# Kernel optimization log

Hardware: AMD Instinct MI355X
Metric: run time of the kernel (lower is better)

The kernel has to match this reference:

```python
import jax, jax.numpy as jnp
import numpy as np

NUM_TYPES = 8
NUM_REL = 6
N_LAYERS = 2


def setup_inputs() -> dict:
    key = jax.random.key(0)
    ks = jax.random.split(key, 8)
    N, E, D_in, D = 20000, 320000, 512, 256
    node_feature = jax.random.normal(ks[0], (N, D_in), dtype=jnp.float32)
    node_type = jax.random.randint(ks[1], (N,), 0, NUM_TYPES)
    edge_index = jax.random.randint(ks[2], (2, E), 0, N)
    edge_type = jax.random.randint(ks[3], (E,), 0, NUM_REL)
    node_position = jnp.arange(N)
    # learned params
    adapt_W = jax.random.normal(ks[4], (NUM_TYPES, D, D_in), dtype=jnp.float32) * 0.02
    adapt_b = jnp.zeros((NUM_TYPES, D), dtype=jnp.float32)
    W_rel = jax.random.normal(ks[5], (N_LAYERS, NUM_REL, D, D), dtype=jnp.float32) * 0.05
    W_self = jax.random.normal(ks[6], (N_LAYERS, D, D), dtype=jnp.float32) * 0.05
    b_self = jnp.zeros((N_LAYERS, D), dtype=jnp.float32)
    return {
        "node_feature": node_feature,
        "node_type": node_type,
        "edge_index": edge_index,
        "edge_type": edge_type,
        "node_position": node_position,
        "adapt_W": adapt_W,
        "adapt_b": adapt_b,
        "W_rel": W_rel,
        "W_self": W_self,
        "b_self": b_self,
    }


def reference(node_feature, node_type, edge_index, edge_type, node_position,
              adapt_W, adapt_b, W_rel, W_self, b_self):
    N = node_feature.shape[0]
    D = adapt_W.shape[1]
    # per-node-type adaptation: res[i] = tanh(W_{t_i} x_i + b_{t_i})
    # (original loops over types with boolean gather/scatter; here we mask-select)
    h = jnp.zeros((N, D), dtype=node_feature.dtype)
    for t in range(NUM_TYPES):
        y = jnp.tanh(node_feature @ adapt_W[t].T + adapt_b[t])
        h = jnp.where((node_type == t)[:, None], y, h)
    # dropout p=0.0 -> identity
    src, dst = edge_index[0], edge_index[1]
    deg = jax.ops.segment_sum(jnp.ones(src.shape, h.dtype), dst, num_segments=N)
    inv_deg = (1.0 / jnp.maximum(deg, 1.0))[:, None]  # [N,1]
    # relational GNN layer stack (stand-in for unseen GraphConv)
    for l in range(N_LAYERS):
        hr = jnp.einsum('nd,rde->rne', h, W_rel[l])      # [R,N,D]
        msg = hr[edge_type, src]                          # [E,D] gather by (relation, src)
        agg = jax.ops.segment_sum(msg, dst, num_segments=N)
        h = jax.nn.relu(agg * inv_deg + h @ W_self[l] + b_self[l])
    return h
```

## Files before the change

kernel.cpp:

```cpp
#include <hip/hip_runtime.h>

constexpr int NTYPES = 8;
constexpr int NREL   = 6;
constexpr int NSLOT  = 7;
constexpr int D      = 256;
constexpr int DIN    = 512;
constexpr int LDH    = NSLOT * D;

using short8 = __attribute__((ext_vector_type(8))) short;
using f32x4  = __attribute__((ext_vector_type(4))) float;

__device__ __forceinline__ ushort f2b(float f) {
  unsigned u = __float_as_uint(f);
  u += 0x7fffu + ((u >> 16) & 1u);
  return (ushort)(u >> 16);
}
__device__ __forceinline__ float b2f(unsigned bits16) {
  return __uint_as_float(bits16 << 16);
}

#define GLOAD_LDS16(g, l)                                              \
  __builtin_amdgcn_global_load_lds(                                    \
      (__attribute__((address_space(1))) void*)(g),                    \
      (__attribute__((address_space(3))) void*)(l), 16, 0, 0)

__global__ void k_zero(int* __restrict__ p, int n) {
  int i = blockIdx.x * blockDim.x + threadIdx.x;
  if (i < n) p[i] = 0;
}

__global__ void k_cvt_bf16(const float* __restrict__ in, ushort* __restrict__ out, int n4) {
  int i = blockIdx.x * blockDim.x + threadIdx.x;
  if (i >= n4) return;
  float4 v = ((const float4*)in)[i];
  ushort4 o;
  o.x = f2b(v.x); o.y = f2b(v.y); o.z = f2b(v.z); o.w = f2b(v.w);
  ((ushort4*)out)[i] = o;
}

__global__ void k_pack_wcat(const float* __restrict__ Wrel, const float* __restrict__ Wself,
                            ushort* __restrict__ Wcat) {
  int l = blockIdx.z, s = blockIdx.y;
  int o = blockIdx.x * 256 + threadIdx.x;
  int e = o >> 8, d = o & 255;
  float v = (s < NREL) ? Wrel[(((size_t)l * NREL + s) * D + d) * D + e]
                       : Wself[((size_t)l * D + d) * D + e];
  Wcat[(((size_t)l * NSLOT + s) * D + e) * D + d] = f2b(v);
}

__global__ void k_type_blockcnt(const int* __restrict__ ntype, int* __restrict__ blockcnt,
                                int N) {
  __shared__ int cnt[NTYPES];
  int i = blockIdx.x * 256 + threadIdx.x;
  if (threadIdx.x < NTYPES) cnt[threadIdx.x] = 0;
  __syncthreads();
  int t = (i < N) ? ntype[i] : -1;
#pragma unroll
  for (int ty = 0; ty < NTYPES; ++ty) {
    unsigned long long m = __ballot(t == ty);
    if ((threadIdx.x & 63) == 0 && m) atomicAdd(&cnt[ty], __popcll(m));
  }
  __syncthreads();
  if (threadIdx.x < NTYPES) blockcnt[blockIdx.x * NTYPES + threadIdx.x] = cnt[threadIdx.x];
}

__global__ void k_type_scan(const int* __restrict__ blockcnt, int* __restrict__ boffset,
                            int* __restrict__ cnt, int* __restrict__ offt, int nb) {
  __shared__ int tot[NTYPES];
  __shared__ int base[NTYPES];
  int t = threadIdx.x;
  if (t < NTYPES) {
    int s = 0;
    for (int b = 0; b < nb; ++b) {
      boffset[b * NTYPES + t] = s;
      s += blockcnt[b * NTYPES + t];
    }
    tot[t] = s;
    cnt[t] = s;
  }
  __syncthreads();
  if (t == 0) {
    int s = 0;
    for (int ty = 0; ty < NTYPES; ++ty) { base[ty] = s; offt[ty] = s; s += tot[ty]; }
  }
  __syncthreads();
  if (t < NTYPES)
    for (int b = 0; b < nb; ++b) boffset[b * NTYPES + t] += base[t];
}

__global__ void k_type_scatter(const int* __restrict__ ntype, const int* __restrict__ boffset,
                               int* __restrict__ perm, int N) {
  __shared__ int cur[NTYPES];
  int i = blockIdx.x * 256 + threadIdx.x;
  if (threadIdx.x < NTYPES) cur[threadIdx.x] = boffset[blockIdx.x * NTYPES + threadIdx.x];
  __syncthreads();
  int t = (i < N) ? ntype[i] : -1;
  int lane = threadIdx.x & 63;
#pragma unroll
  for (int ty = 0; ty < NTYPES; ++ty) {
    unsigned long long m = __ballot(t == ty);
    if (m) {
      int wbase = 0;
      if (lane == 0) wbase = atomicAdd(&cur[ty], __popcll(m));
      wbase = __shfl(wbase, 0);
      if (t == ty) {
        int rank = __popcll(m & ((1ull << lane) - 1ull));
        perm[wbase + rank] = i;
      }
    }
  }
}

__global__ void k_degree(const int* __restrict__ dst, int* deg, int E) {
  int i = blockIdx.x * blockDim.x + threadIdx.x;
  if (i < E) atomicAdd(&deg[dst[i]], 1);
}

__global__ void k_scan_block(const int* __restrict__ deg, int* __restrict__ rowptr,
                             int* __restrict__ bsum, int N) {
  __shared__ int s[256];
  int i = blockIdx.x * 256 + threadIdx.x;
  int v = (i < N) ? deg[i] : 0;
  s[threadIdx.x] = v;
  __syncthreads();
  for (int o = 1; o < 256; o <<= 1) {
    int t = (threadIdx.x >= o) ? s[threadIdx.x - o] : 0;
    __syncthreads();
    s[threadIdx.x] += t;
    __syncthreads();
  }
  if (i < N) rowptr[i] = s[threadIdx.x] - v;
  if (threadIdx.x == 255) bsum[blockIdx.x] = s[255];
}
__global__ void k_scan_bsum(int* bsum, int nb) {
  if (threadIdx.x == 0) {
    int s = 0;
    for (int b = 0; b < nb; ++b) { int t = bsum[b]; bsum[b] = s; s += t; }
  }
}
__global__ void k_scan_add(int* __restrict__ rowptr, int* __restrict__ cursor,
                           const int* __restrict__ bsum, const int* __restrict__ deg,
                           float* __restrict__ inv, int N, int E) {
  int i = blockIdx.x * 256 + threadIdx.x;
  if (i < N) {
    int r = rowptr[i] + bsum[blockIdx.x];
    rowptr[i] = r;
    cursor[i] = r;
    inv[i] = 1.0f / fmaxf((float)deg[i], 1.0f);
  }
  if (i == 0) rowptr[N] = E;
}
__global__ void k_sortedges(const int* __restrict__ src, const int* __restrict__ dst,
                            const int* __restrict__ et, int* cursor,
                            int* __restrict__ epack, int E) {
  int e = blockIdx.x * 256 + threadIdx.x;
  if (e < E) {
    int pos = atomicAdd(&cursor[dst[e]], 1);
    epack[pos] = (src[e] << 3) | et[e];
  }
}

template <int BM, int BN, int NTN, int KDIM, bool ADAPT, int OCC>
__global__ __launch_bounds__(256, OCC)
void k_mfma_gemm(const ushort* __restrict__ A, const ushort* __restrict__ B,
                 const float* __restrict__ bias,
                 const int* __restrict__ perm, const int* __restrict__ cnt,
                 const int* __restrict__ off,
                 ushort* __restrict__ Cout, int N, int ldC) {
  const int nwg = gridDim.x;
  const int qq = nwg >> 3, rr = nwg & 7;
  const int xcd = blockIdx.x & 7, idx = blockIdx.x >> 3;
  const int wgid = (xcd < rr ? xcd * (qq + 1) : rr * (qq + 1) + (xcd - rr) * qq) + idx;

  int mcnt = N, mtile, ntile;
  const int* permt = nullptr;
  const ushort* Bt = B;
  const float* biast = bias;
  if (ADAPT) {
    const int mt = nwg / (NTYPES * NTN);
    const int t = wgid / (mt * NTN);
    const int rem = wgid % (mt * NTN);
    mtile = rem / NTN;
    ntile = rem % NTN;
    mcnt = cnt[t];
    permt = perm + off[t];
    Bt = B + (size_t)t * D * KDIM;
    biast = bias + t * D;
  } else {
    mtile = wgid / NTN;
    ntile = wgid % NTN;
  }
  const int m0 = mtile * BM;
  if (m0 >= mcnt) return;
  const int n0 = ntile * BN;

  __shared__ ushort SM[2][2][BM * 32];
  static_assert(BM * BN <= 2 * 2 * BM * 32, "C tile must fit in staging LDS");

  const int tid  = threadIdx.x;
  const int lane = tid & 63;
  const int w    = tid >> 6;
  constexpr int FR = BM / 32;
  constexpr int FC = BN / 32;
  const int wr   = (w >> 1) * (BM / 2);
  const int wc   = (w & 1) * (BN / 2);

  constexpr int PW = BM / 16 / 4;
  const ushort* gA[PW];
  const ushort* gB[PW];
  int lo[PW];
#pragma unroll
  for (int u = 0; u < PW; ++u) {
    const int c  = w + u * 4;
    const int r  = c * 16 + (lane >> 2);
    const int sl = (lane & 3) ^ ((r >> 1) & 3);
    int ga;
    if (ADAPT) ga = permt[min(m0 + r, mcnt - 1)];
    else       ga = min(m0 + r, N - 1);
    gA[u] = A + (size_t)ga * KDIM + sl * 8;
    gB[u] = Bt + (size_t)(n0 + r) * KDIM + sl * 8;
    lo[u] = c * 512;
  }

  auto STAGE = [&](int k0, int buf) {
#pragma unroll
    for (int u = 0; u < PW; ++u) {
      GLOAD_LDS16(gA[u] + k0, &SM[buf][0][lo[u]]);
      GLOAD_LDS16(gB[u] + k0, &SM[buf][1][lo[u]]);
    }
  };

  f32x4 acc[FR][FC] = {};

  const int r15 = lane & 15;
  const int g   = lane >> 4;
  const int gsw = g ^ ((r15 >> 1) & 3);

  STAGE(0, 0);
  __syncthreads();

  constexpr int NT = KDIM / 32;
  int curb = 0;
#pragma unroll
  for (int kt = 0; kt < NT; ++kt) {
    if (kt + 1 < NT) STAGE((kt + 1) * 32, curb ^ 1);

    short8 af[FR], bf[FC];
#pragma unroll
    for (int i = 0; i < FR; ++i)
      af[i] = *(const short8*)(&SM[curb][0][(wr + i * 16 + r15) * 32 + gsw * 8]);
#pragma unroll
    for (int j = 0; j < FC; ++j)
      bf[j] = *(const short8*)(&SM[curb][1][(wc + j * 16 + r15) * 32 + gsw * 8]);
#pragma unroll
    for (int i = 0; i < FR; ++i)
#pragma unroll
      for (int j = 0; j < FC; ++j)
        acc[i][j] = __builtin_amdgcn_mfma_f32_16x16x32_bf16(af[i], bf[j], acc[i][j], 0, 0, 0);

    __syncthreads();
    curb ^= 1;
  }

  ushort* Ct = (ushort*)SM;
#pragma unroll
  for (int i = 0; i < FR; ++i) {
#pragma unroll
    for (int q4 = 0; q4 < 4; ++q4) {
      const int row = wr + i * 16 + (lane >> 4) * 4 + q4;
#pragma unroll
      for (int j = 0; j < FC; ++j) {
        const int col = wc + j * 16 + r15;
        float v = acc[i][j][q4];
        if (ADAPT) v = tanhf(v + biast[n0 + col]);
        Ct[row * BN + col] = f2b(v);
      }
    }
  }
  __syncthreads();
  constexpr int C8 = BN / 8;
  constexpr int UNITS = BM * C8;
#pragma unroll
  for (int u0 = 0; u0 < UNITS; u0 += 256) {
    const int u = u0 + tid;
    const int row = u / C8, c8 = u % C8;
    const int rl = m0 + row;
    if (rl < mcnt) {
      const int grow = ADAPT ? permt[rl] : rl;
      *(short8*)(Cout + (size_t)grow * ldC + n0 + c8 * 8) =
          *(const short8*)(Ct + row * BN + c8 * 8);
    }
  }
}

template <bool LAST>
__global__ void k_combine(const ushort* __restrict__ Hall, const int* __restrict__ rowptr,
                          const int* __restrict__ epack, const float* __restrict__ invd,
                          const float* __restrict__ bias, void* __restrict__ outp, int N) {
  int v = blockIdx.x * 4 + (threadIdx.x >> 6);
  if (v >= N) return;
  int lane = threadIdx.x & 63;
  int e0 = rowptr[v], e1 = rowptr[v + 1];
  const uint2 s = *(const uint2*)(Hall + (size_t)v * LDH + NREL * D + lane * 4);
  float iv = invd[v];
  const float4 b4 = *(const float4*)(bias + lane * 4);

  float a0 = 0.f, a1 = 0.f, a2 = 0.f, a3 = 0.f;
  int e = e0;
  for (; e + 8 <= e1; e += 8) {
    uint2 u[8];
#pragma unroll
    for (int k = 0; k < 8; ++k) {
      int p = epack[e + k];
      u[k] = *(const uint2*)(Hall + (size_t)(p >> 3) * LDH + (p & 7) * D + lane * 4);
    }
#pragma unroll
    for (int k = 0; k < 8; ++k) {
      a0 += b2f(u[k].x & 0xffffu);
      a1 += __uint_as_float(u[k].x & 0xffff0000u);
      a2 += b2f(u[k].y & 0xffffu);
      a3 += __uint_as_float(u[k].y & 0xffff0000u);
    }
  }
  if (e + 4 <= e1) {
    uint2 u[4];
#pragma unroll
    for (int k = 0; k < 4; ++k) {
      int p = epack[e + k];
      u[k] = *(const uint2*)(Hall + (size_t)(p >> 3) * LDH + (p & 7) * D + lane * 4);
    }
#pragma unroll
    for (int k = 0; k < 4; ++k) {
      a0 += b2f(u[k].x & 0xffffu);
      a1 += __uint_as_float(u[k].x & 0xffff0000u);
      a2 += b2f(u[k].y & 0xffffu);
      a3 += __uint_as_float(u[k].y & 0xffff0000u);
    }
    e += 4;
  }
  for (; e < e1; ++e) {
    int p = epack[e];
    const uint2 u = *(const uint2*)(Hall + (size_t)(p >> 3) * LDH + (p & 7) * D + lane * 4);
    a0 += b2f(u.x & 0xffffu);
    a1 += __uint_as_float(u.x & 0xffff0000u);
    a2 += b2f(u.y & 0xffffu);
    a3 += __uint_as_float(u.y & 0xffff0000u);
  }
  float o0 = fmaxf(fmaf(a0, iv, b2f(s.x & 0xffffu)) + b4.x, 0.f);
  float o1 = fmaxf(fmaf(a1, iv, __uint_as_float(s.x & 0xffff0000u)) + b4.y, 0.f);
  float o2 = fmaxf(fmaf(a2, iv, b2f(s.y & 0xffffu)) + b4.z, 0.f);
  float o3 = fmaxf(fmaf(a3, iv, __uint_as_float(s.y & 0xffff0000u)) + b4.w, 0.f);
  if (LAST) {
    float4 o; o.x = o0; o.y = o1; o.z = o2; o.w = o3;
    ((float4*)outp)[(size_t)v * 64 + lane] = o;
  } else {
    ushort4 o; o.x = f2b(o0); o.y = f2b(o1); o.z = f2b(o2); o.w = f2b(o3);
    ((ushort4*)outp)[(size_t)v * 64 + lane] = o;
  }
}

extern "C" void kernel_launch(void* const* d_in, const int* in_sizes, int n_in,
                              void* d_out, int out_size, void* d_ws, size_t ws_size,
                              hipStream_t stream) {
  const float* X       = (const float*)d_in[0];
  const int*   ntype   = (const int*)d_in[1];
  const int*   eidx    = (const int*)d_in[2];
  const int*   etype   = (const int*)d_in[3];
  const float* adapt_W = (const float*)d_in[5];
  const float* adapt_b = (const float*)d_in[6];
  const float* W_rel   = (const float*)d_in[7];
  const float* W_self  = (const float*)d_in[8];
  const float* b_self  = (const float*)d_in[9];

  const int N = in_sizes[1];
  const int E = in_sizes[3];
  const int* src = eidx;
  const int* dst = eidx + E;

  char* ws = (char*)d_ws;
  size_t o = 0;
  auto alloc = [&](size_t bytes) { void* p = ws + o; o += (bytes + 255) & ~255ull; return p; };

  ushort* Hall  = (ushort*)alloc((size_t)N * LDH * 2);
  ushort* Xb    = Hall;
  ushort* h     = (ushort*)alloc((size_t)N * D * 2);
  ushort* Wab   = (ushort*)alloc((size_t)NTYPES * D * DIN * 2);
  ushort* Wcat  = (ushort*)alloc((size_t)2 * NSLOT * D * D * 2);
  int*   deg    = (int*)alloc((size_t)N * 4);
  float* inv    = (float*)alloc((size_t)N * 4);
  int*   perm   = (int*)alloc((size_t)N * 4);
  int*   rowptr = (int*)alloc((size_t)(N + 1) * 4);
  int*   cursor = (int*)alloc((size_t)N * 4);
  int*   epack  = (int*)alloc((size_t)E * 4);
  int*   bsum   = (int*)alloc(1024 * 4);
  int*   blockcnt = (int*)alloc((size_t)1024 * NTYPES * 4);
  int*   boffset  = (int*)alloc((size_t)1024 * NTYPES * 4);
  int*   cnt    = (int*)alloc(NTYPES * 4);
  int*   offt   = (int*)alloc(NTYPES * 4);

  const int thr = 256;
  const int nbN = (N + thr - 1) / thr;
  const int nbE = (E + thr - 1) / thr;

  k_zero<<<nbN, thr, 0, stream>>>(deg, N);

  k_cvt_bf16<<<(N * DIN / 4 + thr - 1) / thr, thr, 0, stream>>>(X, Xb, N * DIN / 4);
  k_cvt_bf16<<<(NTYPES * D * DIN / 4 + thr - 1) / thr, thr, 0, stream>>>(adapt_W, Wab,
                                                                          NTYPES * D * DIN / 4);
  dim3 gW(D * D / 256, NSLOT, 2);
  k_pack_wcat<<<gW, 256, 0, stream>>>(W_rel, W_self, Wcat);

  k_type_blockcnt<<<nbN, thr, 0, stream>>>(ntype, blockcnt, N);
  k_type_scan<<<1, 64, 0, stream>>>(blockcnt, boffset, cnt, offt, nbN);
  k_type_scatter<<<nbN, thr, 0, stream>>>(ntype, boffset, perm, N);
  k_degree<<<nbE, thr, 0, stream>>>(dst, deg, E);

  k_scan_block<<<nbN, 256, 0, stream>>>(deg, rowptr, bsum, N);
  k_scan_bsum<<<1, 64, 0, stream>>>(bsum, nbN);
  k_scan_add<<<nbN, 256, 0, stream>>>(rowptr, cursor, bsum, deg, inv, N, E);
  k_sortedges<<<nbE, 256, 0, stream>>>(src, dst, etype, cursor, epack, E);

  const int mtA = (N + 63) / 64;
  const int nwgA = NTYPES * mtA * (D / 64);
  k_mfma_gemm<64, 64, D / 64, DIN, true, 6><<<nwgA, 256, 0, stream>>>(
      Xb, Wab, adapt_b, perm, cnt, offt, h, N, D);

  const int mtL = (N + 127) / 128;
  const int nwgL = mtL * (LDH / 128);
  for (int l = 0; l < 2; ++l) {
    const ushort* Wl = Wcat + (size_t)l * NSLOT * D * D;
    k_mfma_gemm<128, 128, LDH / 128, D, false, 4><<<nwgL, 256, 0, stream>>>(
        h, Wl, nullptr, nullptr, nullptr, nullptr, Hall, N, LDH);
    if (l == 0)
      k_combine<false><<<(N + 3) / 4, 256, 0, stream>>>(Hall, rowptr, epack, inv,
                                                        b_self + (size_t)l * D, h, N);
    else
      k_combine<true><<<(N + 3) / 4, 256, 0, stream>>>(Hall, rowptr, epack, inv,
                                                       b_self + (size_t)l * D, d_out, N);
  }
}
```

Baseline: 231.1 us.

## Aggregate neighbors per relation before transform, then one K=1792 GEMM

Reorders each GNN layer from transform-then-gather to gather-then-transform. A new aggregate kernel sums bf16 neighbor features per relation into a [N, 7*256] buffer scaled by inverse degree, with the self features in the last slot. A single GEMM against concatenated weights (K=1792, output 256) then applies bias and ReLU in its epilogue. This cuts the gather width from a 1792-wide Hall row to a 256-wide h row and removes the separate combine pass. The cost is 6 per-relation accumulators in registers, with a branch on relation type per edge, and a GEMM with a longer K.

```diff
diff --git a/kernel.cpp b/kernel.cpp
--- a/kernel.cpp
+++ b/kernel.cpp
@@ -38,14 +38,15 @@
   ((ushort4*)out)[i] = o;
 }
 
-__global__ void k_pack_wcat(const float* __restrict__ Wrel, const float* __restrict__ Wself,
-                            ushort* __restrict__ Wcat) {
-  int l = blockIdx.z, s = blockIdx.y;
-  int o = blockIdx.x * 256 + threadIdx.x;
-  int e = o >> 8, d = o & 255;
-  float v = (s < NREL) ? Wrel[(((size_t)l * NREL + s) * D + d) * D + e]
-                       : Wself[((size_t)l * D + d) * D + e];
-  Wcat[(((size_t)l * NSLOT + s) * D + e) * D + d] = f2b(v);
+__global__ void k_pack_wcat2(const float* __restrict__ Wrel, const float* __restrict__ Wself,
+                             ushort* __restrict__ W2) {
+  int l = blockIdx.y;
+  int idx = blockIdx.x * 256 + threadIdx.x;
+  int e = idx / LDH, k = idx % LDH;
+  float v = (k < NREL * D)
+                ? Wrel[(((size_t)l * NREL + (k >> 8)) * D + (k & 255)) * D + e]
+                : Wself[((size_t)l * D + (k - NREL * D)) * D + e];
+  W2[((size_t)l * D + e) * LDH + k] = f2b(v);
 }
 
 __global__ void k_type_blockcnt(const int* __restrict__ ntype, int* __restrict__ blockcnt,
@@ -160,13 +161,65 @@
   }
 }
 
-template <int BM, int BN, int NTN, int KDIM, bool ADAPT, int OCC>
+__global__ void k_aggregate(const ushort* __restrict__ h, const int* __restrict__ rowptr,
+                            const int* __restrict__ epack, const float* __restrict__ invd,
+                            ushort* __restrict__ S, int N) {
+  int v = blockIdx.x * 4 + (threadIdx.x >> 6);
+  if (v >= N) return;
+  int lane = threadIdx.x & 63;
+  float acc[NREL][4] = {};
+  int e0 = rowptr[v], e1 = rowptr[v + 1];
+
+  auto ACC = [&](int p, uint2 u) {
+    float f0 = b2f(u.x & 0xffffu), f1 = __uint_as_float(u.x & 0xffff0000u);
+    float f2 = b2f(u.y & 0xffffu), f3 = __uint_as_float(u.y & 0xffff0000u);
+    int r = __builtin_amdgcn_readfirstlane(p) & 7;
+    switch (r) {
+      case 0: acc[0][0]+=f0; acc[0][1]+=f1; acc[0][2]+=f2; acc[0][3]+=f3; break;
+      case 1: acc[1][0]+=f0; acc[1][1]+=f1; acc[1][2]+=f2; acc[1][3]+=f3; break;
+      case 2: acc[2][0]+=f0; acc[2][1]+=f1; acc[2][2]+=f2; acc[2][3]+=f3; break;
+      case 3: acc[3][0]+=f0; acc[3][1]+=f1; acc[3][2]+=f2; acc[3][3]+=f3; break;
+      case 4: acc[4][0]+=f0; acc[4][1]+=f1; acc[4][2]+=f2; acc[4][3]+=f3; break;
+      default: acc[5][0]+=f0; acc[5][1]+=f1; acc[5][2]+=f2; acc[5][3]+=f3; break;
+    }
+  };
+
+  int e = e0;
+  for (; e + 8 <= e1; e += 8) {
+    int p[8]; uint2 u[8];
+#pragma unroll
+    for (int k = 0; k < 8; ++k) {
+      p[k] = epack[e + k];
+      u[k] = *(const uint2*)(h + (size_t)(p[k] >> 3) * D + lane * 4);
+    }
+#pragma unroll
+    for (int k = 0; k < 8; ++k) ACC(p[k], u[k]);
+  }
+  for (; e < e1; ++e) {
+    int p = epack[e];
+    uint2 u = *(const uint2*)(h + (size_t)(p >> 3) * D + lane * 4);
+    ACC(p, u);
+  }
+
+  float iv = invd[v];
+#pragma unroll
+  for (int r = 0; r < NREL; ++r) {
+    ushort4 o;
+    o.x = f2b(acc[r][0] * iv); o.y = f2b(acc[r][1] * iv);
+    o.z = f2b(acc[r][2] * iv); o.w = f2b(acc[r][3] * iv);
+    *(ushort4*)(S + (size_t)v * LDH + r * D + lane * 4) = o;
+  }
+  uint2 sh = *(const uint2*)(h + (size_t)v * D + lane * 4);
+  *(uint2*)(S + (size_t)v * LDH + NREL * D + lane * 4) = sh;
+}
+
+template <int BM, int BN, int NTN, int KDIM, bool ADAPT, int EPI, int OCC>
 __global__ __launch_bounds__(256, OCC)
 void k_mfma_gemm(const ushort* __restrict__ A, const ushort* __restrict__ B,
                  const float* __restrict__ bias,
                  const int* __restrict__ perm, const int* __restrict__ cnt,
                  const int* __restrict__ off,
-                 ushort* __restrict__ Cout, int N, int ldC) {
+                 void* __restrict__ Cout, int N, int ldC) {
   const int nwg = gridDim.x;
   const int qq = nwg >> 3, rr = nwg & 7;
   const int xcd = blockIdx.x & 7, idx = blockIdx.x >> 3;
@@ -195,7 +248,7 @@
   const int n0 = ntile * BN;
 
   __shared__ ushort SM[2][2][BM * 32];
-  static_assert(BM * BN <= 2 * 2 * BM * 32, "C tile must fit in staging LDS");
+  static_assert(EPI == 2 || BM * BN <= 2 * 2 * BM * 32, "C tile must fit staging LDS");
 
   const int tid  = threadIdx.x;
   const int lane = tid & 63;
@@ -231,131 +284,84 @@
   };
 
   f32x4 acc[FR][FC] = {};
-
   const int r15 = lane & 15;
   const int g   = lane >> 4;
   const int gsw = g ^ ((r15 >> 1) & 3);
 
-  STAGE(0, 0);
-  __syncthreads();
-
   constexpr int NT = KDIM / 32;
-  int curb = 0;
-#pragma unroll
-  for (int kt = 0; kt < NT; ++kt) {
-    if (kt + 1 < NT) STAGE((kt + 1) * 32, curb ^ 1);
-
+  static_assert((NT & 1) == 0, "paired double-buffer needs even NT");
+
+  auto KSTEP = [&](int kt, int buf) {
+    if (kt + 1 < NT) STAGE((kt + 1) * 32, buf ^ 1);
     short8 af[FR], bf[FC];
 #pragma unroll
     for (int i = 0; i < FR; ++i)
-      af[i] = *(const short8*)(&SM[curb][0][(wr + i * 16 + r15) * 32 + gsw * 8]);
+      af[i] = *(const short8*)(&SM[buf][0][(wr + i * 16 + r15) * 32 + gsw * 8]);
 #pragma unroll
     for (int j = 0; j < FC; ++j)
-      bf[j] = *(const short8*)(&SM[curb][1][(wc + j * 16 + r15) * 32 + gsw * 8]);
+      bf[j] = *(const short8*)(&SM[buf][1][(wc + j * 16 + r15) * 32 + gsw * 8]);
 #pragma unroll
     for (int i = 0; i < FR; ++i)
 #pragma unroll
       for (int j = 0; j < FC; ++j)
         acc[i][j] = __builtin_amdgcn_mfma_f32_16x16x32_bf16(af[i], bf[j], acc[i][j], 0, 0, 0);
-
     __syncthreads();
-    curb ^= 1;
-  }
-
-  ushort* Ct = (ushort*)SM;
-#pragma unroll
-  for (int i = 0; i < FR; ++i) {
-#pragma unroll
-    for (int q4 = 0; q4 < 4; ++q4) {
-      const int row = wr + i * 16 + (lane >> 4) * 4 + q4;
-#pragma unroll
-      for (int j = 0; j < FC; ++j) {
-        const int col = wc + j * 16 + r15;
-        float v = acc[i][j][q4];
-        if (ADAPT) v = tanhf(v + biast[n0 + col]);
-        Ct[row * BN + col] = f2b(v);
+  };
+
+  STAGE(0, 0);
+  __syncthreads();
+  for (int kt2 = 0; kt2 < NT / 2; ++kt2) {
+    KSTEP(2 * kt2, 0);
+    KSTEP(2 * kt2 + 1, 1);
+  }
+
+  if constexpr (EPI == 2) {
+    float* Co = (float*)Cout;
+#pragma unroll
+    for (int i = 0; i < FR; ++i) {
+#pragma unroll
+      for (int q4 = 0; q4 < 4; ++q4) {
+        const int m = m0 + wr + i * 16 + (lane >> 4) * 4 + q4;
+        if (m < N) {
+#pragma unroll
+          for (int j = 0; j < FC; ++j) {
+            const int n = n0 + wc + j * 16 + r15;
+            Co[(size_t)m * ldC + n] = fmaxf(acc[i][j][q4] + biast[n], 0.0f);
+          }
+        }
       }
     }
-  }
-  __syncthreads();
-  constexpr int C8 = BN / 8;
-  constexpr int UNITS = BM * C8;
-#pragma unroll
-  for (int u0 = 0; u0 < UNITS; u0 += 256) {
-    const int u = u0 + tid;
-    const int row = u / C8, c8 = u % C8;
-    const int rl = m0 + row;
-    if (rl < mcnt) {
-      const int grow = ADAPT ? permt[rl] : rl;
-      *(short8*)(Cout + (size_t)grow * ldC + n0 + c8 * 8) =
-          *(const short8*)(Ct + row * BN + c8 * 8);
-    }
-  }
-}
-
-template <bool LAST>
-__global__ void k_combine(const ushort* __restrict__ Hall, const int* __restrict__ rowptr,
-                          const int* __restrict__ epack, const float* __restrict__ invd,
-                          const float* __restrict__ bias, void* __restrict__ outp, int N) {
-  int v = blockIdx.x * 4 + (threadIdx.x >> 6);
-  if (v >= N) return;
-  int lane = threadIdx.x & 63;
-  int e0 = rowptr[v], e1 = rowptr[v + 1];
-  const uint2 s = *(const uint2*)(Hall + (size_t)v * LDH + NREL * D + lane * 4);
-  float iv = invd[v];
-  const float4 b4 = *(const float4*)(bias + lane * 4);
-
-  float a0 = 0.f, a1 = 0.f, a2 = 0.f, a3 = 0.f;
-  int e = e0;
-  for (; e + 8 <= e1; e += 8) {
-    uint2 u[8];
-#pragma unroll
-    for (int k = 0; k < 8; ++k) {
-      int p = epack[e + k];
-      u[k] = *(const uint2*)(Hall + (size_t)(p >> 3) * LDH + (p & 7) * D + lane * 4);
-    }
-#pragma unroll
-    for (int k = 0; k < 8; ++k) {
-      a0 += b2f(u[k].x & 0xffffu);
-      a1 += __uint_as_float(u[k].x & 0xffff0000u);
-      a2 += b2f(u[k].y & 0xffffu);
-      a3 += __uint_as_float(u[k].y & 0xffff0000u);
-    }
-  }
-  if (e + 4 <= e1) {
-    uint2 u[4];
-#pragma unroll
-    for (int k = 0; k < 4; ++k) {
-      int p = epack[e + k];
-      u[k] = *(const uint2*)(Hall + (size_t)(p >> 3) * LDH + (p & 7) * D + lane * 4);
-    }
-#pragma unroll
-    for (int k = 0; k < 4; ++k) {
-      a0 += b2f(u[k].x & 0xffffu);
-      a1 += __uint_as_float(u[k].x & 0xffff0000u);
-      a2 += b2f(u[k].y & 0xffffu);
-      a3 += __uint_as_float(u[k].y & 0xffff0000u);
-    }
-    e += 4;
-  }
-  for (; e < e1; ++e) {
-    int p = epack[e];
-    const uint2 u = *(const uint2*)(Hall + (size_t)(p >> 3) * LDH + (p & 7) * D + lane * 4);
-    a0 += b2f(u.x & 0xffffu);
-    a1 += __uint_as_float(u.x & 0xffff0000u);
-    a2 += b2f(u.y & 0xffffu);
-    a3 += __uint_as_float(u.y & 0xffff0000u);
-  }
-  float o0 = fmaxf(fmaf(a0, iv, b2f(s.x & 0xffffu)) + b4.x, 0.f);
-  float o1 = fmaxf(fmaf(a1, iv, __uint_as_float(s.x & 0xffff0000u)) + b4.y, 0.f);
-  float o2 = fmaxf(fmaf(a2, iv, b2f(s.y & 0xffffu)) + b4.z, 0.f);
-  float o3 = fmaxf(fmaf(a3, iv, __uint_as_float(s.y & 0xffff0000u)) + b4.w, 0.f);
-  if (LAST) {
-    float4 o; o.x = o0; o.y = o1; o.z = o2; o.w = o3;
-    ((float4*)outp)[(size_t)v * 64 + lane] = o;
   } else {
-    ushort4 o; o.x = f2b(o0); o.y = f2b(o1); o.z = f2b(o2); o.w = f2b(o3);
-    ((ushort4*)outp)[(size_t)v * 64 + lane] = o;
+    ushort* Ct = (ushort*)SM;
+#pragma unroll
+    for (int i = 0; i < FR; ++i) {
+#pragma unroll
+      for (int q4 = 0; q4 < 4; ++q4) {
+        const int row = wr + i * 16 + (lane >> 4) * 4 + q4;
+#pragma unroll
+        for (int j = 0; j < FC; ++j) {
+          const int col = wc + j * 16 + r15;
+          float v = acc[i][j][q4];
+          v = (EPI == 0) ? tanhf(v + biast[n0 + col]) : fmaxf(v + biast[n0 + col], 0.0f);
+          Ct[row * BN + col] = f2b(v);
+        }
+      }
+    }
+    __syncthreads();
+    constexpr int C8 = BN / 8;
+    constexpr int UNITS = BM * C8;
+    ushort* Co = (ushort*)Cout;
+#pragma unroll
+    for (int u0 = 0; u0 < UNITS; u0 += 256) {
+      const int u = u0 + tid;
+      const int row = u / C8, c8 = u % C8;
+      const int rl = m0 + row;
+      if (rl < mcnt) {
+        const int grow = ADAPT ? permt[rl] : rl;
+        *(short8*)(Co + (size_t)grow * ldC + n0 + c8 * 8) =
+            *(const short8*)(Ct + row * BN + c8 * 8);
+      }
+    }
   }
 }
 
@@ -381,11 +387,11 @@
   size_t o = 0;
   auto alloc = [&](size_t bytes) { void* p = ws + o; o += (bytes + 255) & ~255ull; return p; };
 
-  ushort* Hall  = (ushort*)alloc((size_t)N * LDH * 2);
-  ushort* Xb    = Hall;
+  ushort* S     = (ushort*)alloc((size_t)N * LDH * 2);
+  ushort* Xb    = S;
   ushort* h     = (ushort*)alloc((size_t)N * D * 2);
   ushort* Wab   = (ushort*)alloc((size_t)NTYPES * D * DIN * 2);
-  ushort* Wcat  = (ushort*)alloc((size_t)2 * NSLOT * D * D * 2);
+  ushort* Wcat2 = (ushort*)alloc((size_t)2 * D * LDH * 2);
   int*   deg    = (int*)alloc((size_t)N * 4);
   float* inv    = (float*)alloc((size_t)N * 4);
   int*   perm   = (int*)alloc((size_t)N * 4);
@@ -407,8 +413,8 @@
   k_cvt_bf16<<<(N * DIN / 4 + thr - 1) / thr, thr, 0, stream>>>(X, Xb, N * DIN / 4);
   k_cvt_bf16<<<(NTYPES * D * DIN / 4 + thr - 1) / thr, thr, 0, stream>>>(adapt_W, Wab,
                                                                           NTYPES * D * DIN / 4);
-  dim3 gW(D * D / 256, NSLOT, 2);
-  k_pack_wcat<<<gW, 256, 0, stream>>>(W_rel, W_self, Wcat);
+  dim3 gW2(D * LDH / 256, 2);
+  k_pack_wcat2<<<gW2, 256, 0, stream>>>(W_rel, W_self, Wcat2);
 
   k_type_blockcnt<<<nbN, thr, 0, stream>>>(ntype, blockcnt, N);
   k_type_scan<<<1, 64, 0, stream>>>(blockcnt, boffset, cnt, offt, nbN);
@@ -422,20 +428,19 @@
 
   const int mtA = (N + 63) / 64;
   const int nwgA = NTYPES * mtA * (D / 64);
-  k_mfma_gemm<64, 64, D / 64, DIN, true, 6><<<nwgA, 256, 0, stream>>>(
+  k_mfma_gemm<64, 64, D / 64, DIN, true, 0, 6><<<nwgA, 256, 0, stream>>>(
       Xb, Wab, adapt_b, perm, cnt, offt, h, N, D);
 
-  const int mtL = (N + 127) / 128;
-  const int nwgL = mtL * (LDH / 128);
+  const int nwgL = mtA * (D / 64);
   for (int l = 0; l < 2; ++l) {
-    const ushort* Wl = Wcat + (size_t)l * NSLOT * D * D;
-    k_mfma_gemm<128, 128, LDH / 128, D, false, 4><<<nwgL, 256, 0, stream>>>(
-        h, Wl, nullptr, nullptr, nullptr, nullptr, Hall, N, LDH);
+    k_aggregate<<<(N + 3) / 4, 256, 0, stream>>>(h, rowptr, epack, inv, S, N);
+    const ushort* Wl = Wcat2 + (size_t)l * D * LDH;
+    const float* bl = b_self + (size_t)l * D;
     if (l == 0)
-      k_combine<false><<<(N + 3) / 4, 256, 0, stream>>>(Hall, rowptr, epack, inv,
-                                                        b_self + (size_t)l * D, h, N);
+      k_mfma_gemm<64, 64, D / 64, LDH, false, 1, 6><<<nwgL, 256, 0, stream>>>(
+          S, Wl, bl, nullptr, nullptr, nullptr, h, N, D);
     else
-      k_combine<true><<<(N + 3) / 4, 256, 0, stream>>>(Hall, rowptr, epack, inv,
-                                                       b_self + (size_t)l * D, d_out, N);
-  }
-}
+      k_mfma_gemm<64, 64, D / 64, LDH, false, 2, 6><<<nwgL, 256, 0, stream>>>(
+          S, Wl, bl, nullptr, nullptr, nullptr, d_out, N, D);
+  }
+}
```

Result: slower. 413.6 us (+78.9%).
